# Kernel tuning notes

Measured on AMD Instinct MI355X. Metric: run time of the kernel, lower is better.

The kernel has to match this reference:

```python
import jax, jax.numpy as jnp
import numpy as np

N_INST, BATCH, IN_DIM, L_DIM = 256, 128, 1024, 512

def setup_inputs() -> dict:
    key = jax.random.key(0)
    k1, k2, k3, k4 = jax.random.split(key, 4)
    # glorot-uniform-ish scales
    sv = np.sqrt(6.0 / (IN_DIM + L_DIM)).astype(np.float32)
    sw = np.sqrt(6.0 / (L_DIM + 1)).astype(np.float32)
    x = jax.random.normal(k1, (N_INST, BATCH, IN_DIM), dtype=jnp.float32)
    v = jax.random.uniform(k2, (IN_DIM, L_DIM), minval=-sv, maxval=sv, dtype=jnp.float32)
    u = jax.random.uniform(k3, (IN_DIM, L_DIM), minval=-sv, maxval=sv, dtype=jnp.float32)
    w = jax.random.uniform(k4, (L_DIM, 1), minval=-sw, maxval=sw, dtype=jnp.float32)
    return {"x": x, "v": v, "u": u, "w": w}

def reference(x, v, u, w):
    # x: [n_instances, batch, in_dim]
    # Fused batched version of the per-instance loop:
    # score_i = (tanh(x_i @ v) * sigmoid(x_i @ u)) @ w, softmax over instances.
    h = jnp.tanh(jnp.einsum('nbd,dl->nbl', x, v))          # [n, b, l]
    g = jax.nn.sigmoid(jnp.einsum('nbd,dl->nbl', x, u))    # [n, b, l]
    scores = jnp.einsum('nbl,lo->nbo', h * g, w)            # [n, b, 1]
    alpha = jax.nn.softmax(scores, axis=0)                  # softmax over instance axis
    return alpha
```

## Files before the change

### kernel.cpp

```cpp
#include <hip/hip_runtime.h>
#include <stdint.h>

typedef unsigned int  u32;
typedef unsigned short u16;
typedef __bf16 v8bf __attribute__((ext_vector_type(8)));
typedef float  v4f  __attribute__((ext_vector_type(4)));

#define N_INST 256
#define BATCH  128
#define IN_DIM 1024
#define L_DIM  512
#define M_TOT  (N_INST*BATCH)
#define NSLICE 16

#define XB_BYTES   ((size_t)M_TOT * IN_DIM * 2)
#define WPK_BYTES  ((size_t)1024 * IN_DIM * 2)

__device__ inline u32 f2bf_pk(float a, float b){
  u32 ua = __builtin_bit_cast(u32, a);
  u32 ub = __builtin_bit_cast(u32, b);
  ua = (ua + 0x7FFFu + ((ua >> 16) & 1u)) >> 16;
  ub = (ub + 0x7FFFu + ((ub >> 16) & 1u)) & 0xFFFF0000u;
  return ua | ub;
}

__device__ inline void gl2lds16(const u16* g, u16* l){
  __builtin_amdgcn_global_load_lds(
      (const __attribute__((address_space(1))) u32*)(g),
      (__attribute__((address_space(3))) u32*)(l), 16, 0, 0);
}

#define PREP_XBLKS 16384
__global__ void prep(const float* __restrict__ x, const float* __restrict__ v,
                     const float* __restrict__ u, u16* __restrict__ xb,
                     u16* __restrict__ wpk){
  const int b = blockIdx.x;
  if (b < PREP_XBLKS){
    int t = b * 256 + threadIdx.x;
    int r = t >> 6, l = t & 63;
    int kk = r & 1, i = (r >> 1) & 3, h = (r >> 3) & 1, kt = (r >> 4) & 15, mb = r >> 8;
    int q = l >> 4, c = l & 15;
    int row = mb*128 + h*64 + i*16 + c;
    int k0  = kt*64 + kk*32 + q*8;
    const float* src = x + (size_t)row * IN_DIM + k0;
    float4 a0 = *reinterpret_cast<const float4*>(src);
    float4 a1 = *reinterpret_cast<const float4*>(src + 4);
    uint4 out;
    out.x = f2bf_pk(a0.x, a0.y); out.y = f2bf_pk(a0.z, a0.w);
    out.z = f2bf_pk(a1.x, a1.y); out.w = f2bf_pk(a1.z, a1.w);
    *reinterpret_cast<uint4*>(xb + (size_t)r*512 + l*8) = out;
  } else {
    int t = (b - PREP_XBLKS) * 256 + threadIdx.x;
    int r = t >> 6, l = t & 63;
    int kk = r & 1, j = (r >> 1) & 3, kt = (r >> 3) & 15, cs = r >> 7;
    int q = l >> 4, c = l & 15;
    int bcol = cs*4 + j;
    const float* src = (bcol & 1) ? u : v;
    int lcol = (bcol >> 1)*16 + c;
    int k0 = kt*64 + kk*32 + q*8;
    u32 o[4];
#pragma unroll
    for (int ii = 0; ii < 4; ++ii){
      float a  = src[(size_t)(k0 + 2*ii    ) * L_DIM + lcol];
      float bb = src[(size_t)(k0 + 2*ii + 1) * L_DIM + lcol];
      o[ii] = f2bf_pk(a, bb);
    }
    *reinterpret_cast<uint4*>(wpk + (size_t)r*512 + l*8) = make_uint4(o[0], o[1], o[2], o[3]);
  }
}

#define LOADA(KT, B_) { const u16* ak_ = awave + (size_t)(KT)*8192;                 \
  _Pragma("unroll") for (int gi_ = 0; gi_ < 4; ++gi_)                               \
    _Pragma("unroll") for (int kk_ = 0; kk_ < 2; ++kk_)                             \
      afb[B_][gi_][kk_] = *reinterpret_cast<const v8bf*>(ak_ + gi_*1024 + kk_*512); }

#define LOADB(KTL, B_) {                                                            \
  _Pragma("unroll") for (int j_ = 0; j_ < 4; ++j_)                                  \
    _Pragma("unroll") for (int kk_ = 0; kk_ < 2; ++kk_)                             \
      bfb[B_][j_][kk_] = *reinterpret_cast<const v8bf*>(&Bs[((KTL)*8 + j_*2 + kk_)*512 + lane*8]); }

#define DOMFMA(B_) {                                                                \
  _Pragma("unroll") for (int kk_ = 0; kk_ < 2; ++kk_)                               \
    _Pragma("unroll") for (int gi_ = 0; gi_ < 4; ++gi_)                             \
      _Pragma("unroll") for (int j_ = 0; j_ < 4; ++j_)                              \
        acc[gi_][j_] = __builtin_amdgcn_mfma_f32_16x16x32_bf16(                     \
            afb[B_][gi_][kk_], bfb[B_][j_][kk_], acc[gi_][j_], 0, 0, 0); }

__launch_bounds__(256, 2)
__global__ void gemm_score(const u16* __restrict__ xb, const u16* __restrict__ wpk,
                           const float* __restrict__ w, float* __restrict__ partial){
  __shared__ __align__(16) u16 Bs[64 * 512];

  const int tid  = threadIdx.x;
  const u32 bid  = blockIdx.x;
  const int xcd  = bid & 7;
  const int slot = bid >> 3;
  const int cs   = slot & 15;
  const int mr   = xcd*16 + (slot >> 4);
  const int mblk0= mr * 2;

  const int lane = tid & 63;
  const int wave = tid >> 6;
  const int q    = lane >> 4;
  const int c    = lane & 15;

  auto stageB = [&](int kh){
    const u16* src = wpk + (size_t)(cs*128 + kh*64) * 512;
#pragma unroll
    for (int it = 0; it < 16; ++it){
      const int rl = wave*16 + it;
      gl2lds16(src + (size_t)rl*512 + lane*8, &Bs[rl*512 + lane*8]);
    }
  };

  const u16* awave = xb + (size_t)(mblk0 + (wave>>1))*131072
                        + (size_t)((wave&1)*4)*1024 + lane*8;

  v8bf afb[2][4][2];
  v8bf bfb[2][4][2];
  v4f  acc[4][4];
#pragma unroll
  for (int gi = 0; gi < 4; ++gi)
#pragma unroll
    for (int j = 0; j < 4; ++j)
      acc[gi][j] = (v4f){0.f, 0.f, 0.f, 0.f};

  stageB(0);
  LOADA(0, 0);
  __syncthreads();
  LOADB(0, 0);

#pragma unroll 1
  for (int k2 = 0; k2 < 4; ++k2){
    const int kt = 2*k2;
    LOADA(kt+1, 1); LOADB(2*k2+1, 1);
    DOMFMA(0);
    LOADA(kt+2, 0);
    if (k2 < 3) LOADB(2*k2+2, 0);
    DOMFMA(1);
  }
  __syncthreads();
  stageB(1);
  __syncthreads();
  LOADB(0, 0);

#pragma unroll 1
  for (int k2 = 0; k2 < 4; ++k2){
    const int kt = 8 + 2*k2;
    LOADA(kt+1, 1); LOADB(2*k2+1, 1);
    DOMFMA(0);
    if (k2 < 3){ LOADA(kt+2, 0); LOADB(2*k2+2, 0); }
    DOMFMA(1);
  }

  const float wl0 = w[cs*32 + c];
  const float wl1 = w[cs*32 + 16 + c];
  float* pout = partial + (size_t)cs * M_TOT
              + (size_t)(mblk0 + (wave>>1))*128 + (wave&1)*64;

#pragma unroll
  for (int gi = 0; gi < 4; ++gi){
#pragma unroll
    for (int r = 0; r < 4; ++r){
      float t0 = 2.f / (1.f + __expf(-2.f * acc[gi][0][r])) - 1.f;
      float s0 = 1.f / (1.f + __expf(-acc[gi][1][r]));
      float t1 = 2.f / (1.f + __expf(-2.f * acc[gi][2][r])) - 1.f;
      float s1 = 1.f / (1.f + __expf(-acc[gi][3][r]));
      float v2 = t0*s0*wl0 + t1*s1*wl1;
      v2 += __shfl_xor(v2, 1, 64);
      v2 += __shfl_xor(v2, 2, 64);
      v2 += __shfl_xor(v2, 4, 64);
      v2 += __shfl_xor(v2, 8, 64);
      if (c == 0) pout[gi*16 + q*4 + r] = v2;
    }
  }
}

__global__ void softmax_inst(const float* __restrict__ partial, float* __restrict__ out){
  __shared__ float red[N_INST];
  const int b = blockIdx.x;
  const int n = threadIdx.x;
  float s = 0.f;
#pragma unroll
  for (int i = 0; i < NSLICE; ++i) s += partial[(size_t)i * M_TOT + n*BATCH + b];
  red[n] = s; __syncthreads();
  for (int st = N_INST/2; st > 0; st >>= 1){
    if (n < st) red[n] = fmaxf(red[n], red[n + st]);
    __syncthreads();
  }
  float mx = red[0]; __syncthreads();
  float e = __expf(s - mx);
  red[n] = e; __syncthreads();
  for (int st = N_INST/2; st > 0; st >>= 1){
    if (n < st) red[n] += red[n + st];
    __syncthreads();
  }
  out[n*BATCH + b] = e / red[0];
}

extern "C" void kernel_launch(void* const* d_in, const int* in_sizes, int n_in,
                              void* d_out, int out_size, void* d_ws, size_t ws_size,
                              hipStream_t stream) {
  const float* x = (const float*)d_in[0];
  const float* v = (const float*)d_in[1];
  const float* u = (const float*)d_in[2];
  const float* w = (const float*)d_in[3];
  u16*   xb      = (u16*)d_ws;
  u16*   wpk     = (u16*)((char*)d_ws + XB_BYTES);
  float* partial = (float*)((char*)d_ws + XB_BYTES + WPK_BYTES);
  float* out     = (float*)d_out;

  prep<<<dim3(PREP_XBLKS + 512), dim3(256), 0, stream>>>(x, v, u, xb, wpk);
  gemm_score<<<dim3(2048), dim3(256), 0, stream>>>(xb, wpk, w, partial);
  softmax_inst<<<dim3(BATCH), dim3(N_INST), 0, stream>>>(partial, out);
}
```

Measured before the change: 288.1 us.

## Double GEMM N-tile per block and double-buffer B staging in LDS

Each block now covers two column slices (64 output columns, 128 B columns) instead of one, halving the grid and the number of partial slices. Every A fragment loaded from global memory therefore feeds twice as many MFMAs, which halves the re-reads of the large bf16 activation matrix. B tiles are staged into two LDS buffers in 16-row chunks per step, so the next chunk loads while the current one is computed. The cost is more accumulator registers (acc grows to 4x8), which risks spills or lower occupancy under launch_bounds(256,2), plus a barrier in every k-step.

```diff
diff --git a/kernel.cpp b/kernel.cpp
--- a/kernel.cpp
+++ b/kernel.cpp
@@ -11,7 +11,7 @@
 #define IN_DIM 1024
 #define L_DIM  512
 #define M_TOT  (N_INST*BATCH)
-#define NSLICE 16
+#define NSLICE 8
 
 #define XB_BYTES   ((size_t)M_TOT * IN_DIM * 2)
 #define WPK_BYTES  ((size_t)1024 * IN_DIM * 2)
@@ -69,34 +69,33 @@
   }
 }
 
-#define LOADA(KT, B_) { const u16* ak_ = awave + (size_t)(KT)*8192;                 \
-  _Pragma("unroll") for (int gi_ = 0; gi_ < 4; ++gi_)                               \
-    _Pragma("unroll") for (int kk_ = 0; kk_ < 2; ++kk_)                             \
-      afb[B_][gi_][kk_] = *reinterpret_cast<const v8bf*>(ak_ + gi_*1024 + kk_*512); }
-
-#define LOADB(KTL, B_) {                                                            \
-  _Pragma("unroll") for (int j_ = 0; j_ < 4; ++j_)                                  \
-    _Pragma("unroll") for (int kk_ = 0; kk_ < 2; ++kk_)                             \
-      bfb[B_][j_][kk_] = *reinterpret_cast<const v8bf*>(&Bs[((KTL)*8 + j_*2 + kk_)*512 + lane*8]); }
-
-#define DOMFMA(B_) {                                                                \
-  _Pragma("unroll") for (int kk_ = 0; kk_ < 2; ++kk_)                               \
-    _Pragma("unroll") for (int gi_ = 0; gi_ < 4; ++gi_)                             \
-      _Pragma("unroll") for (int j_ = 0; j_ < 4; ++j_)                              \
-        acc[gi_][j_] = __builtin_amdgcn_mfma_f32_16x16x32_bf16(                     \
-            afb[B_][gi_][kk_], bfb[B_][j_][kk_], acc[gi_][j_], 0, 0, 0); }
+
+#define LOADA_K(KT, KK, B_) { const u16* ak_ = awave + (size_t)(KT)*8192 + (KK)*512;  \
+  _Pragma("unroll") for (int gi_ = 0; gi_ < 4; ++gi_)                                 \
+    afb[B_][gi_] = *reinterpret_cast<const v8bf*>(ak_ + gi_*1024); }
+
+#define LOADB_K(BUF, KTL, KK, B_) {                                                   \
+  _Pragma("unroll") for (int j_ = 0; j_ < 8; ++j_)                                    \
+    bfb[B_][j_] = *reinterpret_cast<const v8bf*>(                                     \
+      &Bs[BUF][(((j_>>2)*16) + (KTL)*8 + ((j_&3)*2) + (KK))*512 + lane*8]); }
+
+#define DOMFMA_K(B_) {                                                                \
+  _Pragma("unroll") for (int gi_ = 0; gi_ < 4; ++gi_)                                 \
+    _Pragma("unroll") for (int j_ = 0; j_ < 8; ++j_)                                  \
+      acc[gi_][j_] = __builtin_amdgcn_mfma_f32_16x16x32_bf16(                         \
+          afb[B_][gi_], bfb[B_][j_], acc[gi_][j_], 0, 0, 0); }
 
 __launch_bounds__(256, 2)
 __global__ void gemm_score(const u16* __restrict__ xb, const u16* __restrict__ wpk,
                            const float* __restrict__ w, float* __restrict__ partial){
-  __shared__ __align__(16) u16 Bs[64 * 512];
+  __shared__ __align__(16) u16 Bs[2][32*512];
 
   const int tid  = threadIdx.x;
   const u32 bid  = blockIdx.x;
   const int xcd  = bid & 7;
   const int slot = bid >> 3;
-  const int cs   = slot & 15;
-  const int mr   = xcd*16 + (slot >> 4);
+  const int csp  = slot & 7;
+  const int mr   = xcd*16 + (slot >> 3);
   const int mblk0= mr * 2;
 
   const int lane = tid & 63;
@@ -104,58 +103,52 @@
   const int q    = lane >> 4;
   const int c    = lane & 15;
 
-  auto stageB = [&](int kh){
-    const u16* src = wpk + (size_t)(cs*128 + kh*64) * 512;
-#pragma unroll
-    for (int it = 0; it < 16; ++it){
-      const int rl = wave*16 + it;
-      gl2lds16(src + (size_t)rl*512 + lane*8, &Bs[rl*512 + lane*8]);
+  auto stageB = [&](int s, int buf){
+#pragma unroll
+    for (int it = 0; it < 8; ++it){
+      const int rr     = wave*8 + it;
+      const int cs_loc = rr >> 4;
+      const int rem    = rr & 15;
+      const u16* src = wpk + ((size_t)((csp*2 + cs_loc)*128 + s*16 + rem))*512 + lane*8;
+      gl2lds16(src, &Bs[buf][rr*512 + lane*8]);
     }
   };
 
   const u16* awave = xb + (size_t)(mblk0 + (wave>>1))*131072
                         + (size_t)((wave&1)*4)*1024 + lane*8;
 
-  v8bf afb[2][4][2];
-  v8bf bfb[2][4][2];
-  v4f  acc[4][4];
+  v8bf afb[2][4];
+  v8bf bfb[2][8];
+  v4f  acc[4][8];
 #pragma unroll
   for (int gi = 0; gi < 4; ++gi)
 #pragma unroll
-    for (int j = 0; j < 4; ++j)
+    for (int j = 0; j < 8; ++j)
       acc[gi][j] = (v4f){0.f, 0.f, 0.f, 0.f};
 
-  stageB(0);
-  LOADA(0, 0);
+  stageB(0, 0);
   __syncthreads();
-  LOADB(0, 0);
+  LOADA_K(0, 0, 0);
+  LOADB_K(0, 0, 0, 0);
 
 #pragma unroll 1
-  for (int k2 = 0; k2 < 4; ++k2){
-    const int kt = 2*k2;
-    LOADA(kt+1, 1); LOADB(2*k2+1, 1);
-    DOMFMA(0);
-    LOADA(kt+2, 0);
-    if (k2 < 3) LOADB(2*k2+2, 0);
-    DOMFMA(1);
-  }
-  __syncthreads();
-  stageB(1);
-  __syncthreads();
-  LOADB(0, 0);
-
-#pragma unroll 1
-  for (int k2 = 0; k2 < 4; ++k2){
-    const int kt = 8 + 2*k2;
-    LOADA(kt+1, 1); LOADB(2*k2+1, 1);
-    DOMFMA(0);
-    if (k2 < 3){ LOADA(kt+2, 0); LOADB(2*k2+2, 0); }
-    DOMFMA(1);
-  }
-
-  const float wl0 = w[cs*32 + c];
-  const float wl1 = w[cs*32 + 16 + c];
-  float* pout = partial + (size_t)cs * M_TOT
+  for (int s = 0; s < 8; ++s){
+    const int cur = s & 1;
+    if (s < 7) stageB(s+1, cur^1);
+    LOADA_K(2*s,   1, 1); LOADB_K(cur, 0, 1, 1); DOMFMA_K(0);
+    LOADA_K(2*s+1, 0, 0); LOADB_K(cur, 1, 0, 0); DOMFMA_K(1);
+    LOADA_K(2*s+1, 1, 1); LOADB_K(cur, 1, 1, 1); DOMFMA_K(0);
+    if (s < 7) LOADA_K(2*s+2, 0, 0);
+    DOMFMA_K(1);
+    __syncthreads();
+    if (s < 7) LOADB_K(cur^1, 0, 0, 0);
+  }
+
+  const float wl0 = w[csp*64 +      c];
+  const float wl1 = w[csp*64 + 16 + c];
+  const float wl2 = w[csp*64 + 32 + c];
+  const float wl3 = w[csp*64 + 48 + c];
+  float* pout = partial + (size_t)csp * M_TOT
               + (size_t)(mblk0 + (wave>>1))*128 + (wave&1)*64;
 
 #pragma unroll
@@ -166,7 +159,11 @@
       float s0 = 1.f / (1.f + __expf(-acc[gi][1][r]));
       float t1 = 2.f / (1.f + __expf(-2.f * acc[gi][2][r])) - 1.f;
       float s1 = 1.f / (1.f + __expf(-acc[gi][3][r]));
-      float v2 = t0*s0*wl0 + t1*s1*wl1;
+      float t2 = 2.f / (1.f + __expf(-2.f * acc[gi][4][r])) - 1.f;
+      float s2 = 1.f / (1.f + __expf(-acc[gi][5][r]));
+      float t3 = 2.f / (1.f + __expf(-2.f * acc[gi][6][r])) - 1.f;
+      float s3 = 1.f / (1.f + __expf(-acc[gi][7][r]));
+      float v2 = t0*s0*wl0 + t1*s1*wl1 + t2*s2*wl2 + t3*s3*wl3;
       v2 += __shfl_xor(v2, 1, 64);
       v2 += __shfl_xor(v2, 2, 64);
       v2 += __shfl_xor(v2, 4, 64);
@@ -211,6 +208,6 @@
   float* out     = (float*)d_out;
 
   prep<<<dim3(PREP_XBLKS + 512), dim3(256), 0, stream>>>(x, v, u, xb, wpk);
-  gemm_score<<<dim3(2048), dim3(256), 0, stream>>>(xb, wpk, w, partial);
+  gemm_score<<<dim3(1024), dim3(256), 0, stream>>>(xb, wpk, w, partial);
   softmax_inst<<<dim3(BATCH), dim3(N_INST), 0, stream>>>(partial, out);
 }
```

After: 304.6 us. +5.7%, slower.
